# Performance work log

Measured on AMD Instinct MI355X. Metric: run time of the kernel, lower is better.

Reference implementation:

```python
import jax, jax.numpy as jnp
import numpy as np
import math

HIDDEN = 2048
NUM_HEADS = 16
HEAD_DIM = 128
ROPE_BASE = 10000.0


def _rope_emb(seq_len, dim, dtype):
    # freqs[i, j] = i * base**(-2j/dim); emb = concat(freqs, freqs) -> [S, dim]
    inv_freq = 1.0 / (ROPE_BASE ** (jnp.arange(0, dim, 2, dtype=jnp.float32) / dim))
    t = jnp.arange(seq_len, dtype=jnp.float32)
    freqs = t[:, None] * inv_freq[None, :]            # [S, dim/2]
    return jnp.concatenate([freqs, freqs], axis=-1).astype(dtype)  # [S, dim]


def _apply_rope(x, emb):
    # x: [B, H, S, D]; emb: [S, D] broadcast over batch and heads.
    # Roll-based rotary variant from the source: x*cos + roll(x, 1, -1)*sin
    e = emb[None, None, :, :]
    return x * jnp.cos(e) + jnp.roll(x, shift=1, axis=-1) * jnp.sin(e)


def setup_inputs() -> dict:
    key = jax.random.key(0)
    ks = jax.random.split(key, 5)
    B, S = 2, 2048
    scale = 1.0 / math.sqrt(HIDDEN)
    return {
        "hidden_states": jax.random.normal(ks[0], (B, S, HIDDEN), dtype=jnp.float32),
        "Wq": jax.random.normal(ks[1], (HIDDEN, HIDDEN), dtype=jnp.float32) * scale,
        "Wk": jax.random.normal(ks[2], (HIDDEN, HIDDEN), dtype=jnp.float32) * scale,
        "Wv": jax.random.normal(ks[3], (HIDDEN, HIDDEN), dtype=jnp.float32) * scale,
        "Wo": jax.random.normal(ks[4], (HIDDEN, HIDDEN), dtype=jnp.float32) * scale,
    }


def reference(hidden_states, Wq, Wk, Wv, Wo):
    B, S, _ = hidden_states.shape
    H, D = NUM_HEADS, HEAD_DIM

    def split_heads(x):
        return x.reshape(B, S, H, D).transpose(0, 2, 1, 3)  # [B,H,S,D]

    q = split_heads(hidden_states @ Wq)
    k = split_heads(hidden_states @ Wk)
    v = split_heads(hidden_states @ Wv)

    emb = _rope_emb(S, D, hidden_states.dtype)  # [S, D]
    q = _apply_rope(q, emb)
    k = _apply_rope(k, emb)

    scores = jnp.einsum("bhqd,bhkd->bhqk", q, k) / math.sqrt(D)  # [B,H,S,S]
    probs = jax.nn.softmax(scores, axis=-1)
    ctx = jnp.einsum("bhqk,bhkd->bhqd", probs, v)  # [B,H,S,D]
    ctx = ctx.transpose(0, 2, 1, 3).reshape(B, S, H * D)
    return ctx @ Wo
```

## Files before the change

### kernel.cpp

```cpp
#include <hip/hip_runtime.h>

#define HIDDEN 2048
#define SEQ    2048
#define BATCH  2
#define NHEAD  16
#define HDIM   128

typedef __attribute__((ext_vector_type(4))) int    i32x4;
typedef __attribute__((ext_vector_type(4))) float  f32x4;
typedef __attribute__((ext_vector_type(8))) __bf16 bf16x8;

__device__ __forceinline__ unsigned short f2bf(float f) {
    return __builtin_bit_cast(unsigned short, (__bf16)f);
}
__device__ __forceinline__ float bf2f(unsigned short h) {
    unsigned u = ((unsigned)h) << 16;
    return __builtin_bit_cast(float, u);
}
__device__ __forceinline__ void gl_lds16(const unsigned short* g, unsigned short* l) {
    __builtin_amdgcn_global_load_lds(
        (const __attribute__((address_space(1))) unsigned int*)g,
        (__attribute__((address_space(3))) unsigned int*)l, 16, 0, 0);
}

__global__ void k_cvt_tables(const float* __restrict__ in, unsigned short* __restrict__ out,
                             float* __restrict__ ctab, float* __restrict__ stab) {
    int bid = blockIdx.x;
    if (bid < 8192) {
        int idx = bid * 256 + threadIdx.x;
        float4 v = ((const float4*)in)[idx];
        ushort4 o;
        o.x = f2bf(v.x); o.y = f2bf(v.y); o.z = f2bf(v.z); o.w = f2bf(v.w);
        ((ushort4*)out)[idx] = o;
    } else {
        int idx = (bid - 8192) * 256 + threadIdx.x;
        int t = idx >> 6, i = idx & 63;
        float inv = expf(-(float)i * 0.14391156831212793f);
        float ang = (float)t * inv;
        ctab[idx] = cosf(ang);
        stab[idx] = sinf(ang);
    }
}

__global__ void k_transcvt4(const float* __restrict__ W0, const float* __restrict__ W1,
                            const float* __restrict__ W2, const float* __restrict__ W3,
                            unsigned short* __restrict__ O0, unsigned short* __restrict__ O1,
                            unsigned short* __restrict__ O2, unsigned short* __restrict__ O3) {
    __shared__ float tile[32][33];
    int z = blockIdx.z;
    const float* in = (z == 0) ? W0 : (z == 1) ? W1 : (z == 2) ? W2 : W3;
    unsigned short* out = (z == 0) ? O0 : (z == 1) ? O1 : (z == 2) ? O2 : O3;
    float scl = (z == 0) ? 0.12751743f : 1.0f;
    int tx = threadIdx.x, ty = threadIdx.y;
    int x = blockIdx.x * 32 + tx, y0 = blockIdx.y * 32;
#pragma unroll
    for (int i = 0; i < 4; i++)
        tile[ty + i * 8][tx] = in[(size_t)(y0 + ty + i * 8) * HIDDEN + x];
    __syncthreads();
    int x2 = blockIdx.y * 32 + tx, y2 = blockIdx.x * 32;
#pragma unroll
    for (int i = 0; i < 4; i++)
        out[(size_t)(y2 + ty + i * 8) * HIDDEN + x2] = f2bf(tile[tx][ty + i * 8] * scl);
}

template <int OUTB>
__global__ __launch_bounds__(512, 1) void k_gemm256(
    const unsigned short* __restrict__ A,
    const unsigned short* __restrict__ B0, const unsigned short* __restrict__ B1,
    const unsigned short* __restrict__ B2,
    void* __restrict__ C0, void* __restrict__ C1, void* __restrict__ C2,
    const float* __restrict__ ctab, const float* __restrict__ stab,
    int K)
{
    __shared__ __align__(16) unsigned short S[3 * 24576];
    const int nwg = gridDim.x;
    int id = blockIdx.x;
    int wg = (id & 7) * (nwg >> 3) + (id >> 3);
    const int z = wg >> 8;
    const int my = (wg >> 4) & 15, nx = wg & 15;
    const unsigned short* Bm = (z == 0) ? B0 : (z == 1 ? B1 : B2);
    void* Cv = (z == 0) ? C0 : (z == 1 ? C1 : C2);
    const int m0 = my * 256, n0 = nx * 128;
    const int tid = threadIdx.x, l = tid & 63, w = tid >> 6;
    const int wm = w >> 1, wn = w & 1;
    const int lr = l & 15, lg = l >> 4;

    const unsigned short* sg[6];
    int so[6];
#pragma unroll
    for (int j = 0; j < 4; j++) {
        int c = tid + j * 512, row = c >> 3, k8 = c & 7;
        sg[j] = A + (size_t)(m0 + row) * K + ((k8 ^ (row & 7)) * 8);
        so[j] = row * 64 + k8 * 8;
    }
#pragma unroll
    for (int j = 0; j < 2; j++) {
        int c = tid + j * 512, row = c >> 3, k8 = c & 7;
        sg[4 + j] = Bm + (size_t)(n0 + row) * K + ((k8 ^ (row & 7)) * 8);
        so[4 + j] = 16384 + row * 64 + k8 * 8;
    }

    f32x4 acc[4][4] = {};

    auto stage = [&](int t) {
        unsigned short* buf = &S[(t % 3) * 24576];
        const int ko = t * 64;
#pragma unroll
        for (int j = 0; j < 6; j++) gl_lds16(sg[j] + ko, &buf[so[j]]);
    };
    auto compute = [&](int t) {
        const unsigned short* buf = &S[(t % 3) * 24576];
        const unsigned short* bb = buf + 16384;
        const int xk0 = (lg ^ (lr & 7)) * 8, xk1 = ((4 + lg) ^ (lr & 7)) * 8;
        i32x4 af0[4], af1[4], bf0[4], bf1[4];
#pragma unroll
        for (int i = 0; i < 4; i++) {
            int R = (wm * 64 + i * 16 + lr) * 64;
            af0[i] = *(const i32x4*)&buf[R + xk0];
            af1[i] = *(const i32x4*)&buf[R + xk1];
        }
#pragma unroll
        for (int j = 0; j < 4; j++) {
            int R = (wn * 64 + j * 16 + lr) * 64;
            bf0[j] = *(const i32x4*)&bb[R + xk0];
            bf1[j] = *(const i32x4*)&bb[R + xk1];
        }
        __builtin_amdgcn_s_setprio(1);
#pragma unroll
        for (int i = 0; i < 4; i++)
#pragma unroll
            for (int j = 0; j < 4; j++)
                acc[i][j] = __builtin_amdgcn_mfma_f32_16x16x32_bf16(
                    __builtin_bit_cast(bf16x8, af0[i]),
                    __builtin_bit_cast(bf16x8, bf0[j]), acc[i][j], 0, 0, 0);
#pragma unroll
        for (int i = 0; i < 4; i++)
#pragma unroll
            for (int j = 0; j < 4; j++)
                acc[i][j] = __builtin_amdgcn_mfma_f32_16x16x32_bf16(
                    __builtin_bit_cast(bf16x8, af1[i]),
                    __builtin_bit_cast(bf16x8, bf1[j]), acc[i][j], 0, 0, 0);
        __builtin_amdgcn_s_setprio(0);
    };

    const int nt = K / 64;
    stage(0); stage(1);
    for (int t = 0; t < nt - 1; ++t) {
        asm volatile("s_waitcnt vmcnt(6)" ::: "memory");
        __builtin_amdgcn_s_barrier();
        __builtin_amdgcn_sched_barrier(0);
        if (t < nt - 2) stage(t + 2);
        compute(t);
    }
    asm volatile("s_waitcnt vmcnt(0)" ::: "memory");
    __builtin_amdgcn_s_barrier();
    __builtin_amdgcn_sched_barrier(0);
    compute(nt - 1);

    if (OUTB && z == 2) {
        unsigned short* Vt = (unsigned short*)Cv;
        const int bb_ = m0 >> 11;
        const int tb = (m0 & 2047) + wm * 64;
#pragma unroll
        for (int i = 0; i < 4; i++)
#pragma unroll
            for (int j = 0; j < 4; j++) {
                int t0 = tb + i * 16 + lg * 4;
                int n = n0 + wn * 64 + j * 16 + lr;
                ushort4 pk;
                pk.x = f2bf(acc[i][j][0]); pk.y = f2bf(acc[i][j][1]);
                pk.z = f2bf(acc[i][j][2]); pk.w = f2bf(acc[i][j][3]);
                *(ushort4*)&Vt[((size_t)(bb_ * 2048 + n)) * 2048 + t0] = pk;
            }
    } else if (OUTB) {
        float* xch = (float*)S;
        if (lr == 15) {
#pragma unroll
            for (int i = 0; i < 4; i++)
#pragma unroll
                for (int r = 0; r < 4; r++)
                    xch[(((wm << 1) | wn) * 4 + i) * 16 + lg * 4 + r] = acc[i][3][r];
        }
        __syncthreads();
        unsigned short* Co = (unsigned short*)Cv;
#pragma unroll
        for (int i = 0; i < 4; i++)
#pragma unroll
            for (int r = 0; r < 4; r++) {
                int m = m0 + wm * 64 + i * 16 + lg * 4 + r;
                int t = m & 2047;
                float ldsprev = xch[(((wm << 1) | (wn ^ 1)) * 4 + i) * 16 + lg * 4 + r];
#pragma unroll
                for (int j = 0; j < 4; j++) {
                    float v = acc[i][j][r];
                    float pA = __shfl(v, l - 1);
                    float prev;
                    if (j == 0) {
                        prev = (lr == 0) ? ldsprev : pA;
                    } else {
                        float pB = __shfl(acc[i][j - 1][r], (l & 48) + 15);
                        prev = (lr == 0) ? pB : pA;
                    }
                    float cc = ctab[t * 64 + j * 16 + lr];
                    float ss = stab[t * 64 + j * 16 + lr];
                    int n = n0 + wn * 64 + j * 16 + lr;
                    Co[(size_t)m * 2048 + n] = f2bf(v * cc + prev * ss);
                }
            }
    } else {
#pragma unroll
        for (int i = 0; i < 4; i++)
#pragma unroll
            for (int j = 0; j < 4; j++)
#pragma unroll
                for (int r = 0; r < 4; r++) {
                    int m = m0 + wm * 64 + i * 16 + lg * 4 + r;
                    int n = n0 + wn * 64 + j * 16 + lr;
                    ((float*)Cv)[(size_t)m * 2048 + n] = acc[i][j][r];
                }
    }
}

__global__ __launch_bounds__(512) void k_attn(
    const unsigned short* __restrict__ Q, const unsigned short* __restrict__ K,
    const unsigned short* __restrict__ Vt, unsigned short* __restrict__ ctx)
{
    __shared__ __align__(16) unsigned short Klds[2][64 * 128];
    __shared__ __align__(16) unsigned short Vlds[2][128 * 64];
    __shared__ __align__(16) unsigned short Plds[8][32 * 64];
    const int tid = threadIdx.x, l = tid & 63, w = tid >> 6;
    const int lr = l & 15, lg = l >> 4;
    const int bid = blockIdx.x;
    const int sX = bid >> 3;
    const int bh = (bid & 7) * 4 + (sX >> 3);
    const int q0 = (sX & 7) * 256;
    const int b = bh >> 4, h = bh & 15;

    i32x4 qf[2][4];
#pragma unroll
    for (int qh = 0; qh < 2; qh++) {
        const unsigned short* qbase =
            Q + (size_t)(b * SEQ + q0 + w * 32 + qh * 16 + lr) * HIDDEN + h * HDIM + lg * 8;
#pragma unroll
        for (int c = 0; c < 4; c++) qf[qh][c] = *(const i32x4*)(qbase + c * 32);
    }

    const unsigned short* kg[2];
    const unsigned short* vg[2];
    int kl[2], vl[2];
#pragma unroll
    for (int c = 0; c < 2; c++) {
        int cc = tid + c * 512;
        {   int row = cc >> 4, ch = cc & 15, sch = ch ^ (row & 7);
            kg[c] = K + (size_t)(b * SEQ + row) * HIDDEN + h * HDIM + sch * 8;
            kl[c] = cc * 8; }
        {   int row = cc >> 3, ch = cc & 7, sch = ch ^ (row & 7);
            vg[c] = Vt + (size_t)(bh * HDIM + row) * SEQ + sch * 8;
            vl[c] = cc * 8; }
    }

    auto stage = [&](int t, int bsel) {
        const size_t ko = (size_t)t * 64;
#pragma unroll
        for (int c = 0; c < 2; c++) {
            gl_lds16(kg[c] + ko * HIDDEN, &Klds[bsel][kl[c]]);
            gl_lds16(vg[c] + ko,          &Vlds[bsel][vl[c]]);
        }
    };

    f32x4 acc[2][8] = {};
    float m_run[2] = {-1e30f, -1e30f}, l_run[2] = {0.f, 0.f};

    stage(0, 0);
    const int nt = SEQ / 64;
    for (int t = 0; t < nt; ++t) {
        asm volatile("s_waitcnt vmcnt(0)" ::: "memory");
        __builtin_amdgcn_s_barrier();
        asm volatile("" ::: "memory");
        __builtin_amdgcn_sched_barrier(0);
        if (t + 1 < nt) stage(t + 1, (t + 1) & 1);
        const unsigned short* Kb_ = Klds[t & 1];
        const unsigned short* Vb_ = Vlds[t & 1];

        f32x4 s[4][2];
        __builtin_amdgcn_s_setprio(1);
#pragma unroll
        for (int ks = 0; ks < 4; ks++) {
            s[ks][0] = f32x4{0.f, 0.f, 0.f, 0.f};
            s[ks][1] = f32x4{0.f, 0.f, 0.f, 0.f};
#pragma unroll
            for (int c = 0; c < 4; c++) {
                i32x4 kf = *(const i32x4*)&Kb_[(ks * 16 + lr) * 128 + ((c * 4 + lg) ^ (lr & 7)) * 8];
                s[ks][0] = __builtin_amdgcn_mfma_f32_16x16x32_bf16(
                    __builtin_bit_cast(bf16x8, kf), __builtin_bit_cast(bf16x8, qf[0][c]),
                    s[ks][0], 0, 0, 0);
                s[ks][1] = __builtin_amdgcn_mfma_f32_16x16x32_bf16(
                    __builtin_bit_cast(bf16x8, kf), __builtin_bit_cast(bf16x8, qf[1][c]),
                    s[ks][1], 0, 0, 0);
            }
        }
        __builtin_amdgcn_s_setprio(0);

        float p[2][4][4];
        float fac[2];
        bool need_any = false;
#pragma unroll
        for (int qh = 0; qh < 2; qh++) {
            float mx0 = fmaxf(fmaxf(s[0][qh][0], s[0][qh][1]), fmaxf(s[0][qh][2], s[0][qh][3]));
            float mx1 = fmaxf(fmaxf(s[1][qh][0], s[1][qh][1]), fmaxf(s[1][qh][2], s[1][qh][3]));
            float mx2 = fmaxf(fmaxf(s[2][qh][0], s[2][qh][1]), fmaxf(s[2][qh][2], s[2][qh][3]));
            float mx3 = fmaxf(fmaxf(s[3][qh][0], s[3][qh][1]), fmaxf(s[3][qh][2], s[3][qh][3]));
            float pmax = fmaxf(fmaxf(mx0, mx1), fmaxf(mx2, mx3));
            pmax = fmaxf(pmax, __shfl_xor(pmax, 16));
            pmax = fmaxf(pmax, __shfl_xor(pmax, 32));
            bool need = pmax > m_run[qh] + 8.0f;
            fac[qh] = need ? __builtin_amdgcn_exp2f(m_run[qh] - pmax) : 1.0f;
            float mn = need ? pmax : m_run[qh];
            m_run[qh] = mn;
            float psum = 0.f;
#pragma unroll
            for (int ks = 0; ks < 4; ks++) {
                float e0 = __builtin_amdgcn_exp2f(s[ks][qh][0] - mn);
                float e1 = __builtin_amdgcn_exp2f(s[ks][qh][1] - mn);
                float e2 = __builtin_amdgcn_exp2f(s[ks][qh][2] - mn);
                float e3 = __builtin_amdgcn_exp2f(s[ks][qh][3] - mn);
                p[qh][ks][0] = e0; p[qh][ks][1] = e1;
                p[qh][ks][2] = e2; p[qh][ks][3] = e3;
                psum += (e0 + e1) + (e2 + e3);
            }
            psum += __shfl_xor(psum, 16);
            psum += __shfl_xor(psum, 32);
            l_run[qh] = l_run[qh] * fac[qh] + psum;
            need_any |= need;
        }

        unsigned short* pw = &Plds[w][0];
#pragma unroll
        for (int qh = 0; qh < 2; qh++)
#pragma unroll
            for (int ks = 0; ks < 4; ks++) {
                ushort4 pk;
                pk.x = f2bf(p[qh][ks][0]); pk.y = f2bf(p[qh][ks][1]);
                pk.z = f2bf(p[qh][ks][2]); pk.w = f2bf(p[qh][ks][3]);
                int chunk = ks * 2 + (lg >> 1);
                *(ushort4*)&pw[(qh * 16 + lr) * 64 + ((chunk ^ (lr & 7)) * 8) + (lg & 1) * 4] = pk;
            }

        if (__any((int)need_any)) {
#pragma unroll
            for (int qh = 0; qh < 2; qh++) {
                float facq[4];
#pragma unroll
                for (int r = 0; r < 4; r++) facq[r] = __shfl(fac[qh], lg * 4 + r);
#pragma unroll
                for (int db = 0; db < 8; db++)
#pragma unroll
                    for (int r = 0; r < 4; r++) acc[qh][db][r] *= facq[r];
            }
        }

        __builtin_amdgcn_s_setprio(1);
#pragma unroll
        for (int kk = 0; kk < 2; kk++) {
            i32x4 pf0 = *(const i32x4*)&pw[(lr) * 64 + ((kk * 4 + lg) ^ (lr & 7)) * 8];
            i32x4 pf1 = *(const i32x4*)&pw[(16 + lr) * 64 + ((kk * 4 + lg) ^ (lr & 7)) * 8];
#pragma unroll
            for (int db = 0; db < 8; db++) {
                i32x4 vf = *(const i32x4*)&Vb_[(db * 16 + lr) * 64 + ((kk * 4 + lg) ^ (lr & 7)) * 8];
                acc[0][db] = __builtin_amdgcn_mfma_f32_16x16x32_bf16(
                    __builtin_bit_cast(bf16x8, pf0), __builtin_bit_cast(bf16x8, vf),
                    acc[0][db], 0, 0, 0);
                acc[1][db] = __builtin_amdgcn_mfma_f32_16x16x32_bf16(
                    __builtin_bit_cast(bf16x8, pf1), __builtin_bit_cast(bf16x8, vf),
                    acc[1][db], 0, 0, 0);
            }
        }
        __builtin_amdgcn_s_setprio(0);
    }

#pragma unroll
    for (int qh = 0; qh < 2; qh++) {
        float inv[4];
#pragma unroll
        for (int r = 0; r < 4; r++) inv[r] = 1.0f / __shfl(l_run[qh], lg * 4 + r);
#pragma unroll
        for (int db = 0; db < 8; db++)
#pragma unroll
            for (int r = 0; r < 4; r++) {
                int trow = q0 + w * 32 + qh * 16 + lg * 4 + r;
                ctx[(size_t)(b * SEQ + trow) * HIDDEN + h * HDIM + db * 16 + lr] =
                    f2bf(acc[qh][db][r] * inv[r]);
            }
    }
}

extern "C" void kernel_launch(void* const* d_in, const int* in_sizes, int n_in,
                              void* d_out, int out_size, void* d_ws, size_t ws_size,
                              hipStream_t stream)
{
    (void)in_sizes; (void)n_in; (void)out_size; (void)ws_size;
    const float* X  = (const float*)d_in[0];
    const float* Wq = (const float*)d_in[1];
    const float* Wk = (const float*)d_in[2];
    const float* Wv = (const float*)d_in[3];
    const float* Wo = (const float*)d_in[4];
    float* out = (float*)d_out;
    char* ws = (char*)d_ws;

    unsigned short* Xb  = (unsigned short*)(ws);
    unsigned short* WqT = (unsigned short*)(ws + 16777216);
    unsigned short* WkT = (unsigned short*)(ws + 25165824);
    unsigned short* WvT = (unsigned short*)(ws + 33554432);
    unsigned short* WoT = (unsigned short*)(ws + 41943040);
    unsigned short* Qb  = (unsigned short*)(ws + 50331648);
    unsigned short* Kb  = (unsigned short*)(ws + 67108864);
    unsigned short* Vt  = (unsigned short*)(ws + 100663296);
    unsigned short* Cx  = (unsigned short*)(ws + 117440512);
    float* ctab = (float*)(ws + 134217728);
    float* stab = (float*)(ws + 134742016);

    k_cvt_tables<<<8704, 256, 0, stream>>>(X, Xb, ctab, stab);
    k_transcvt4<<<dim3(64, 64, 4), dim3(32, 8), 0, stream>>>(Wq, Wk, Wv, Wo,
                                                             WqT, WkT, WvT, WoT);
    k_gemm256<1><<<768, 512, 0, stream>>>(Xb, WqT, WkT, WvT, Qb, Kb, Vt,
                                          ctab, stab, 2048);
    k_attn<<<256, 512, 0, stream>>>(Qb, Kb, Vt, Cx);
    k_gemm256<0><<<256, 512, 0, stream>>>(Cx, WoT, WoT, WoT, out, out, out,
                                          nullptr, nullptr, 2048);
}
```

Measured before the change: 261.4 us.

## Triple-buffer attention K/V loads and merge prep kernels into one launch

The attention kernel moves from double- to triple-buffered K/V tiles in LDS. Loads are now issued two tiles ahead, and the kernel waits only for the older tile's loads (vmcnt(4)) instead of draining all of them. Separately, the weight transpose/convert kernel and the input convert/rope-table kernel are merged into a single launch to cut one kernel launch and its tail. The extra LDS buffers raise shared memory use per block, which may reduce occupancy.

```diff
diff --git a/kernel.cpp b/kernel.cpp
--- a/kernel.cpp
+++ b/kernel.cpp
@@ -23,44 +23,45 @@
         (__attribute__((address_space(3))) unsigned int*)l, 16, 0, 0);
 }
 
-__global__ void k_cvt_tables(const float* __restrict__ in, unsigned short* __restrict__ out,
-                             float* __restrict__ ctab, float* __restrict__ stab) {
-    int bid = blockIdx.x;
-    if (bid < 8192) {
-        int idx = bid * 256 + threadIdx.x;
-        float4 v = ((const float4*)in)[idx];
+__global__ void k_prep(const float* __restrict__ X, unsigned short* __restrict__ Xb,
+                       float* __restrict__ ctab, float* __restrict__ stab,
+                       const float* __restrict__ W0, const float* __restrict__ W1,
+                       const float* __restrict__ W2, const float* __restrict__ W3,
+                       unsigned short* __restrict__ O0, unsigned short* __restrict__ O1,
+                       unsigned short* __restrict__ O2, unsigned short* __restrict__ O3)
+{
+    __shared__ float tile[32][33];
+    int bid = blockIdx.x, tid = threadIdx.x;
+    if (bid < 16384) {
+        int z = bid >> 12, rem = bid & 4095;
+        int by = rem >> 6, bx = rem & 63;
+        const float* in = (z == 0) ? W0 : (z == 1) ? W1 : (z == 2) ? W2 : W3;
+        unsigned short* out = (z == 0) ? O0 : (z == 1) ? O1 : (z == 2) ? O2 : O3;
+        float scl = (z == 0) ? 0.12751743f : 1.0f;
+        int tx = tid & 31, ty = tid >> 5;
+        int x = bx * 32 + tx, y0 = by * 32;
+#pragma unroll
+        for (int i = 0; i < 4; i++)
+            tile[ty + i * 8][tx] = in[(size_t)(y0 + ty + i * 8) * HIDDEN + x];
+        __syncthreads();
+        int x2 = by * 32 + tx, y2 = bx * 32;
+#pragma unroll
+        for (int i = 0; i < 4; i++)
+            out[(size_t)(y2 + ty + i * 8) * HIDDEN + x2] = f2bf(tile[tx][ty + i * 8] * scl);
+    } else if (bid < 24576) {
+        int idx = (bid - 16384) * 256 + tid;
+        float4 v = ((const float4*)X)[idx];
         ushort4 o;
         o.x = f2bf(v.x); o.y = f2bf(v.y); o.z = f2bf(v.z); o.w = f2bf(v.w);
-        ((ushort4*)out)[idx] = o;
+        ((ushort4*)Xb)[idx] = o;
     } else {
-        int idx = (bid - 8192) * 256 + threadIdx.x;
+        int idx = (bid - 24576) * 256 + tid;
         int t = idx >> 6, i = idx & 63;
         float inv = expf(-(float)i * 0.14391156831212793f);
         float ang = (float)t * inv;
         ctab[idx] = cosf(ang);
         stab[idx] = sinf(ang);
     }
-}
-
-__global__ void k_transcvt4(const float* __restrict__ W0, const float* __restrict__ W1,
-                            const float* __restrict__ W2, const float* __restrict__ W3,
-                            unsigned short* __restrict__ O0, unsigned short* __restrict__ O1,
-                            unsigned short* __restrict__ O2, unsigned short* __restrict__ O3) {
-    __shared__ float tile[32][33];
-    int z = blockIdx.z;
-    const float* in = (z == 0) ? W0 : (z == 1) ? W1 : (z == 2) ? W2 : W3;
-    unsigned short* out = (z == 0) ? O0 : (z == 1) ? O1 : (z == 2) ? O2 : O3;
-    float scl = (z == 0) ? 0.12751743f : 1.0f;
-    int tx = threadIdx.x, ty = threadIdx.y;
-    int x = blockIdx.x * 32 + tx, y0 = blockIdx.y * 32;
-#pragma unroll
-    for (int i = 0; i < 4; i++)
-        tile[ty + i * 8][tx] = in[(size_t)(y0 + ty + i * 8) * HIDDEN + x];
-    __syncthreads();
-    int x2 = blockIdx.y * 32 + tx, y2 = blockIdx.x * 32;
-#pragma unroll
-    for (int i = 0; i < 4; i++)
-        out[(size_t)(y2 + ty + i * 8) * HIDDEN + x2] = f2bf(tile[tx][ty + i * 8] * scl);
 }
 
 template <int OUTB>
@@ -225,8 +226,8 @@
     const unsigned short* __restrict__ Q, const unsigned short* __restrict__ K,
     const unsigned short* __restrict__ Vt, unsigned short* __restrict__ ctx)
 {
-    __shared__ __align__(16) unsigned short Klds[2][64 * 128];
-    __shared__ __align__(16) unsigned short Vlds[2][128 * 64];
+    __shared__ __align__(16) unsigned short Klds[3][64 * 128];
+    __shared__ __align__(16) unsigned short Vlds[3][128 * 64];
     __shared__ __align__(16) unsigned short Plds[8][32 * 64];
     const int tid = threadIdx.x, l = tid & 63, w = tid >> 6;
     const int lr = l & 15, lg = l >> 4;
@@ -259,7 +260,8 @@
             vl[c] = cc * 8; }
     }
 
-    auto stage = [&](int t, int bsel) {
+    auto stage = [&](int t) {
+        const int bsel = t % 3;
         const size_t ko = (size_t)t * 64;
 #pragma unroll
         for (int c = 0; c < 2; c++) {
@@ -271,16 +273,16 @@
     f32x4 acc[2][8] = {};
     float m_run[2] = {-1e30f, -1e30f}, l_run[2] = {0.f, 0.f};
 
-    stage(0, 0);
+    stage(0); stage(1);
     const int nt = SEQ / 64;
     for (int t = 0; t < nt; ++t) {
-        asm volatile("s_waitcnt vmcnt(0)" ::: "memory");
+        if (t + 1 < nt) { asm volatile("s_waitcnt vmcnt(4)" ::: "memory"); }
+        else            { asm volatile("s_waitcnt vmcnt(0)" ::: "memory"); }
         __builtin_amdgcn_s_barrier();
-        asm volatile("" ::: "memory");
         __builtin_amdgcn_sched_barrier(0);
-        if (t + 1 < nt) stage(t + 1, (t + 1) & 1);
-        const unsigned short* Kb_ = Klds[t & 1];
-        const unsigned short* Vb_ = Vlds[t & 1];
+        if (t + 2 < nt) stage(t + 2);
+        const unsigned short* Kb_ = Klds[t % 3];
+        const unsigned short* Vb_ = Vlds[t % 3];
 
         f32x4 s[4][2];
         __builtin_amdgcn_s_setprio(1);
@@ -419,9 +421,8 @@
     float* ctab = (float*)(ws + 134217728);
     float* stab = (float*)(ws + 134742016);
 
-    k_cvt_tables<<<8704, 256, 0, stream>>>(X, Xb, ctab, stab);
-    k_transcvt4<<<dim3(64, 64, 4), dim3(32, 8), 0, stream>>>(Wq, Wk, Wv, Wo,
-                                                             WqT, WkT, WvT, WoT);
+    k_prep<<<25088, 256, 0, stream>>>(X, Xb, ctab, stab, Wq, Wk, Wv, Wo,
+                                      WqT, WkT, WvT, WoT);
     k_gemm256<1><<<768, 512, 0, stream>>>(Xb, WqT, WkT, WvT, Qb, Kb, Vt,
                                           ctab, stab, 2048);
     k_attn<<<256, 512, 0, stream>>>(Qb, Kb, Vt, Cx);
```

Result: no change. 259.3 us (median of 2 runs) (-0.8%).
